# Performance work log

Hardware: AMD Instinct MI355X
Metric: run time of the kernel (lower is better)

Reference implementation:

```python
import jax, jax.numpy as jnp
import numpy as np

DIM = 64
WS = 8    # window_size
SS = 4    # shift_size


def _conv(x, w, pad, groups=1):
    return jax.lax.conv_general_dilated(
        x, w, (1, 1), ((pad, pad), (pad, pad)),
        dimension_numbers=('NCHW', 'OIHW', 'NCHW'),
        feature_group_count=groups)


def _window_partition(x, ws):
    # x: (B, C, H, W) -> (B*Hn*Wn, C, ws, ws), with bottom/right padding
    B, C, H, W = x.shape
    pb = (-H) % ws
    pr = (-W) % ws
    x = jnp.pad(x, ((0, 0), (0, 0), (0, pb), (0, pr)))
    Hp, Wp = H + pb, W + pr
    x = x.reshape(B, C, Hp // ws, ws, Wp // ws, ws).transpose(0, 1, 2, 4, 3, 5)
    return x.reshape(-1, C, ws, ws)


def _window_reverse(wins, ws, H, W):
    pb = (-H) % ws
    pr = (-W) % ws
    Hp, Wp = H + pb, W + pr
    B = wins.shape[0] // ((Hp // ws) * (Wp // ws))
    x = wins.reshape(B, -1, Hp // ws, Wp // ws, ws, ws).transpose(0, 1, 2, 4, 3, 5)
    x = x.reshape(B, -1, Hp, Wp)
    return x[:, :, :H, :W]


def _create_mask(H, W, ws, ss):
    # Swin-style additive mask, computed statically with numpy
    Hp = int(np.ceil(H / ws)) * ws
    Wp = int(np.ceil(W / ws)) * ws
    m = np.zeros((Hp, Wp), dtype=np.float32)
    slices = (slice(0, -ws), slice(-ws, -ss), slice(-ss, None))
    cnt = 0
    for hs in slices:
        for wsl in slices:
            m[hs, wsl] = cnt
            cnt += 1
    mw = m.reshape(Hp // ws, ws, Wp // ws, ws).transpose(0, 2, 1, 3).reshape(-1, ws * ws)
    diff = mw[:, None, :] - mw[:, :, None]
    return jnp.asarray(np.where(diff != 0, -100.0, 0.0).astype(np.float32))


def _l2norm(x):
    # matches torch F.normalize(dim=-1, eps=1e-12)
    return x / jnp.maximum(jnp.linalg.norm(x, axis=-1, keepdims=True), 1e-12)


def _win_attn(xw, w_qkv, w_dw, w_proj, ws, mask, b):
    # xw: (N, C, ws, ws) windows
    C = xw.shape[1]
    qkv = _conv(_conv(xw, w_qkv, 0), w_dw, 1, groups=3 * C)
    q, k, v = jnp.split(qkv, 3, axis=1)
    N = q.shape[0]
    hw = ws * ws
    q = _l2norm(q.reshape(N, C, hw))
    k = _l2norm(k.reshape(N, C, hw))
    v = v.reshape(N, C, hw)
    attn = jnp.einsum('nci,ncj->nij', q, k) / ws  # (N, hw, hw)
    if mask is not None:
        attn = (attn.reshape(b, -1, hw, hw) + mask[None]).reshape(-1, hw, hw)
    attn = jax.nn.softmax(attn, axis=-1)
    out = jnp.einsum('nci,nij->ncj', v, attn).reshape(N, C, ws, ws)
    return _conv(out, w_proj, 1)


def _forward(x, w_qkv0, w_dw0, w_proj0, w_qkv1, w_dw1, w_proj1):
    b, c, h, w = x.shape
    # pass 1: unshifted windows
    xw = _window_partition(x, WS)
    out = _win_attn(xw, w_qkv0, w_dw0, w_proj0, WS, None, b)
    out = _window_reverse(out, WS, h, w)
    # pass 2: shifted windows with Swin mask
    shift = jnp.roll(out, (-SS, -SS), axis=(2, 3))
    sw = _window_partition(shift, WS)
    mask = _create_mask(h, w, WS, SS)
    out = _win_attn(sw, w_qkv1, w_dw1, w_proj1, WS, mask, b)
    out = _window_reverse(out, WS, h, w)
    return jnp.roll(out, (SS, SS), axis=(2, 3))


def setup_inputs() -> dict:
    key = jax.random.key(0)
    ks = jax.random.split(key, 7)
    C = DIM
    s = 0.05
    return {
        'x': jax.random.normal(ks[0], (8, C, 256, 256), jnp.float32),
        'w_qkv0': jax.random.normal(ks[1], (3 * C, C, 1, 1), jnp.float32) * s,
        'w_dw0': jax.random.normal(ks[2], (3 * C, 1, 3, 3), jnp.float32) * s,
        'w_proj0': jax.random.normal(ks[3], (C, C, 3, 3), jnp.float32) * s,
        'w_qkv1': jax.random.normal(ks[4], (3 * C, C, 1, 1), jnp.float32) * s,
        'w_dw1': jax.random.normal(ks[5], (3 * C, 1, 3, 3), jnp.float32) * s,
        'w_proj1': jax.random.normal(ks[6], (C, C, 3, 3), jnp.float32) * s,
    }


def reference(x, w_qkv0, w_dw0, w_proj0, w_qkv1, w_dw1, w_proj1):
    return _forward(x, w_qkv0, w_dw0, w_proj0, w_qkv1, w_dw1, w_proj1)
```

## Files before the change

### kernel.cpp

```cpp
#include <hip/hip_runtime.h>


typedef __attribute__((ext_vector_type(8))) short bf8;
typedef __attribute__((ext_vector_type(4))) float f32x4;
#define MFMA(a, b, c) __builtin_amdgcn_mfma_f32_16x16x32_bf16(a, b, c, 0, 0, 0)

__device__ __forceinline__ int xkey(int p) { return ((p >> 3) ^ p) & 7; }
__device__ __forceinline__ int xswz(int p, int c) { return p * 64 + (c ^ (xkey(p) << 3)); }
__device__ __forceinline__ int kswz(int r, int c) {
    return r * 32 + (c ^ ((((r >> 3) ^ (r >> 1)) & 3) << 3));
}
__device__ __forceinline__ int sswz(int ch, int p) {
    return ch * 64 + (p ^ (((ch >> 1) & 7) << 2));
}
__device__ __forceinline__ int jswz(int ch, int p) {
    return ch * 64 + (p ^ (((ch >> 1) & 7) << 3));
}

__device__ __forceinline__ unsigned cvtpk(float a, float b) {
    unsigned r;
    asm("v_cvt_pk_bf16_f32 %0, %1, %2" : "=v"(r) : "v"(a), "v"(b));
    return r;
}

__device__ __forceinline__ void bsplit(float f, short& h, short& l) {
    unsigned u = __float_as_uint(f);
    unsigned hb = (u + 0x7FFFu + ((u >> 16) & 1u)) >> 16;
    float hf = __uint_as_float(hb << 16);
    float r = f - hf;
    unsigned u2 = __float_as_uint(r);
    unsigned lb = (u2 + 0x7FFFu + ((u2 >> 16) & 1u)) >> 16;
    h = (short)hb; l = (short)lb;
}
__device__ __forceinline__ void bsplit2(float a, float b, unsigned& hw, unsigned& lw) {
    hw = cvtpk(a, b);
    float ra = a - __uint_as_float(hw << 16);
    float rb = b - __uint_as_float(hw & 0xFFFF0000u);
    lw = cvtpk(ra, rb);
}

__global__ void k_fq(const float* __restrict__ wq, short* __restrict__ oh, short* __restrict__ ol) {
    int bx = blockIdx.x;
    int kk = bx / 12, tt = bx % 12;
    int tid = threadIdx.x;
    int lane = tid >> 3, j = tid & 7;
    int oc = tt * 16 + (lane & 15);
    int ic = kk * 32 + ((lane >> 4) << 3) + j;
    short h, l; bsplit(wq[oc * 64 + ic], h, l);
    oh[bx * 512 + tid] = h; ol[bx * 512 + tid] = l;
}
__global__ void k_fp(const float* __restrict__ wp, short* __restrict__ oh, short* __restrict__ ol) {
    int bx = blockIdx.x;
    int tap = bx >> 3, kk = (bx >> 2) & 1, tt = bx & 3;
    int tid = threadIdx.x;
    int lane = tid >> 3, j = tid & 7;
    int oc = tt * 16 + (lane & 15);
    int ic = kk * 32 + ((lane >> 4) << 3) + j;
    short h, l; bsplit(wp[(oc * 64 + ic) * 9 + tap], h, l);
    oh[bx * 512 + tid] = h; ol[bx * 512 + tid] = l;
}

__device__ __forceinline__ void dw_one(const float* scr, const float* wd,
                                       int ch, int row, float o[8]) {
    float w9[9];
    #pragma unroll
    for (int tp = 0; tp < 9; ++tp) w9[tp] = wd[tp];
    float e[3][10];
    #pragma unroll
    for (int k3 = 0; k3 < 3; ++k3) {
        int rr = row - 1 + k3;
        e[k3][0] = 0.f; e[k3][9] = 0.f;
        if ((unsigned)rr < 8u) {
            float4 a = *(const float4*)&scr[sswz(ch, rr * 8)];
            float4 b = *(const float4*)&scr[sswz(ch, rr * 8 + 4)];
            e[k3][1] = a.x; e[k3][2] = a.y; e[k3][3] = a.z; e[k3][4] = a.w;
            e[k3][5] = b.x; e[k3][6] = b.y; e[k3][7] = b.z; e[k3][8] = b.w;
        } else {
            #pragma unroll
            for (int q2 = 1; q2 < 9; ++q2) e[k3][q2] = 0.f;
        }
    }
    #pragma unroll
    for (int s = 0; s < 8; ++s) {
        float a = 0.f;
        #pragma unroll
        for (int k3 = 0; k3 < 3; ++k3)
            #pragma unroll
            for (int dx = 0; dx < 3; ++dx)
                a = fmaf(w9[k3 * 3 + dx], e[k3][s + dx], a);
        o[s] = a;
    }
}

__device__ __forceinline__ float norm8(const float d[8]) {
    float ss = 0.f;
    #pragma unroll
    for (int s = 0; s < 8; ++s) ss = fmaf(d[s], d[s], ss);
    ss += __shfl_xor(ss, 1); ss += __shfl_xor(ss, 2); ss += __shfl_xor(ss, 4);
    return fmaxf(sqrtf(ss), 1e-12f);
}

__device__ __forceinline__ void p2_chunk32(const short* XTh, const short* XTl,
                                           const short* bqh, const short* bql,
                                           float* scr, int chunk,
                                           int mh, int nh, int col, int quad, int qo8, int lane)
{
    f32x4 acc[2];
    #pragma unroll
    for (int mt = 0; mt < 2; ++mt) acc[mt] = (f32x4){0.f, 0.f, 0.f, 0.f};
    #pragma unroll
    for (int kk = 0; kk < 2; ++kk) {
        bf8 Ah[2], Al[2];
        #pragma unroll
        for (int mt = 0; mt < 2; ++mt) {
            int row = (mh * 2 + mt) * 16 + col;
            int ad = row * 64 + ((kk * 32 + qo8) ^ (xkey(row) << 3));
            Ah[mt] = *(const bf8*)&XTh[ad];
            Al[mt] = *(const bf8*)&XTl[ad];
        }
        int tt = chunk * 2 + nh;
        bf8 Bh = *(const bf8*)&bqh[((kk * 12 + tt) * 64 + lane) * 8];
        bf8 Bl = *(const bf8*)&bql[((kk * 12 + tt) * 64 + lane) * 8];
        #pragma unroll
        for (int mt = 0; mt < 2; ++mt) {
            acc[mt] = MFMA(Ah[mt], Bh, acc[mt]);
            acc[mt] = MFMA(Ah[mt], Bl, acc[mt]);
            acc[mt] = MFMA(Al[mt], Bh, acc[mt]);
        }
    }
    #pragma unroll
    for (int mt = 0; mt < 2; ++mt) {
        int ocl = nh * 16 + col;
        int p0 = (mh * 2 + mt) * 16 + quad * 4;
        *(f32x4*)&scr[sswz(ocl, p0)] = acc[mt];
    }
}

__global__ __launch_bounds__(256, 4)
void k_fused(const float* __restrict__ in,
             const short* __restrict__ bqh, const short* __restrict__ bql,
             const float* __restrict__ wdw,
             const short* __restrict__ bph, const short* __restrict__ bpl,
             float* __restrict__ out, int shift, int use_mask, int roll)
{
    __shared__ __align__(16) char smem[32768];
    short* XTh = (short*)smem;
    short* XTl = (short*)(smem + 8192);
    short* K0h = (short*)(smem + 16384);
    short* K0l = (short*)(smem + 20480);
    short* K1h = (short*)(smem + 24576);
    short* K1l = (short*)(smem + 28672);
    float* scr = (float*)(smem + 24576);
    short* vbh = (short*)(smem + 16384);
    short* vbl = (short*)(smem + 20480);
    short* PTf = (short*)(smem + 24576);
    short* PTg = (short*)(smem + 28672);
    float* projo = (float*)(smem + 16384);

    const int tid = threadIdx.x, lane = tid & 63, wv = tid >> 6;
    const int col = lane & 15, quad = lane >> 4, qo8 = quad * 8;
    const int mh = wv & 1, nh = wv >> 1;
    const int ch = tid >> 3, rrow = tid & 7;
    const int n = blockIdx.x;
    const int b = n >> 10, c = (n >> 4) & 63, t = n & 15;
    const size_t base = ((size_t)(b * 64 + c)) << 16;

    #pragma unroll
    for (int k = 0; k < 16; k += 2) {
        int o0 = tid + k * 256, o1 = o0 + 256;
        int hi0 = o0 >> 11, r0 = (o0 >> 8) & 7, lo0 = (o0 >> 3) & 31, s0 = o0 & 7;
        int hi1 = o1 >> 11, r1 = (o1 >> 8) & 7, lo1 = (o1 >> 3) & 31, s1 = o1 & 7;
        float v0 = in[base + (size_t)(((t * 16 + hi0 * 8 + r0) + shift) & 255) * 256
                           + (((lo0 * 8 + s0) + shift) & 255)];
        float v1 = in[base + (size_t)(((t * 16 + hi1 * 8 + r1) + shift) & 255) * 256
                           + (((lo1 * 8 + s1) + shift) & 255)];
        unsigned hw, lw; bsplit2(v0, v1, hw, lw);
        int ad0 = xswz(r0 * 8 + s0, hi0 * 32 + lo0);
        int ad1 = xswz(r1 * 8 + s1, hi1 * 32 + lo1);
        XTh[ad0] = (short)hw; XTh[ad1] = (short)(hw >> 16);
        XTl[ad0] = (short)lw; XTl[ad1] = (short)(lw >> 16);
    }
    __syncthreads();

    unsigned qAh[4], qAl[4], qBh[4], qBl[4];
    unsigned vAh[4], vAl[4], vBh[4], vBl[4];
    float nqA, nqB;

    p2_chunk32(XTh, XTl, bqh, bql, scr, 0, mh, nh, col, quad, qo8, lane);
    __syncthreads();
    {
        float dq[8];
        dw_one(scr, wdw + ch * 9, ch, rrow, dq);
        nqA = norm8(dq);
        #pragma unroll
        for (int q2 = 0; q2 < 4; ++q2) bsplit2(dq[2 * q2], dq[2 * q2 + 1], qAh[q2], qAl[q2]);
    }
    __syncthreads();
    p2_chunk32(XTh, XTl, bqh, bql, scr, 1, mh, nh, col, quad, qo8, lane);
    __syncthreads();
    {
        float dq[8];
        dw_one(scr, wdw + (32 + ch) * 9, ch, rrow, dq);
        nqB = norm8(dq);
        #pragma unroll
        for (int q2 = 0; q2 < 4; ++q2) bsplit2(dq[2 * q2], dq[2 * q2 + 1], qBh[q2], qBl[q2]);
    }
    __syncthreads();
    p2_chunk32(XTh, XTl, bqh, bql, scr, 4, mh, nh, col, quad, qo8, lane);
    __syncthreads();
    {
        float dv[8];
        dw_one(scr, wdw + (128 + ch) * 9, ch, rrow, dv);
        #pragma unroll
        for (int q2 = 0; q2 < 4; ++q2) bsplit2(dv[2 * q2], dv[2 * q2 + 1], vAh[q2], vAl[q2]);
    }
    __syncthreads();
    p2_chunk32(XTh, XTl, bqh, bql, scr, 5, mh, nh, col, quad, qo8, lane);
    __syncthreads();
    {
        float dv[8];
        dw_one(scr, wdw + (160 + ch) * 9, ch, rrow, dv);
        #pragma unroll
        for (int q2 = 0; q2 < 4; ++q2) bsplit2(dv[2 * q2], dv[2 * q2 + 1], vBh[q2], vBl[q2]);
    }
    __syncthreads();
    p2_chunk32(XTh, XTl, bqh, bql, scr, 2, mh, nh, col, quad, qo8, lane);
    __syncthreads();
    {
        float dk[8];
        dw_one(scr, wdw + (64 + ch) * 9, ch, rrow, dk);
        float sc = 0.125f / (nqA * norm8(dk));
        #pragma unroll
        for (int s = 0; s < 8; ++s) dk[s] *= sc;
        #pragma unroll
        for (int s0 = 0; s0 < 8; s0 += 2) {
            unsigned hw, lw; bsplit2(dk[s0], dk[s0 + 1], hw, lw);
            int p0 = rrow * 8 + s0;
            int a0 = kswz(p0, ch), a1 = kswz(p0 + 1, ch);
            K0h[a0] = (short)hw; K0h[a1] = (short)(hw >> 16);
            K0l[a0] = (short)lw; K0l[a1] = (short)(lw >> 16);
        }
    }
    __syncthreads();
    p2_chunk32(XTh, XTl, bqh, bql, scr, 3, mh, nh, col, quad, qo8, lane);
    __syncthreads();
    unsigned k1h[4], k1l[4];
    {
        float dk[8];
        dw_one(scr, wdw + (96 + ch) * 9, ch, rrow, dk);
        float sc = 0.125f / (nqB * norm8(dk));
        #pragma unroll
        for (int s = 0; s < 8; ++s) dk[s] *= sc;
        #pragma unroll
        for (int q2 = 0; q2 < 4; ++q2) bsplit2(dk[2 * q2], dk[2 * q2 + 1], k1h[q2], k1l[q2]);
    }
    #pragma unroll
    for (int q2 = 0; q2 < 4; ++q2) {
        int p0 = rrow * 8 + 2 * q2;
        int a0 = xswz(p0, ch), a1 = xswz(p0 + 1, ch);
        XTh[a0] = (short)qAh[q2]; XTh[a1] = (short)(qAh[q2] >> 16);
        XTl[a0] = (short)qAl[q2]; XTl[a1] = (short)(qAl[q2] >> 16);
        int cg = 32 + ch;
        int b0 = xswz(p0, cg), b1 = xswz(p0 + 1, cg);
        XTh[b0] = (short)qBh[q2]; XTh[b1] = (short)(qBh[q2] >> 16);
        XTl[b0] = (short)qBl[q2]; XTl[b1] = (short)(qBl[q2] >> 16);
    }
    __syncthreads();
    #pragma unroll
    for (int q2 = 0; q2 < 4; ++q2) {
        int p0 = rrow * 8 + 2 * q2;
        int a0 = kswz(p0, ch), a1 = kswz(p0 + 1, ch);
        K1h[a0] = (short)k1h[q2]; K1h[a1] = (short)(k1h[q2] >> 16);
        K1l[a0] = (short)k1l[q2]; K1l[a1] = (short)(k1l[q2] >> 16);
    }
    __syncthreads();

    f32x4 at[4];
    #pragma unroll
    for (int nt = 0; nt < 4; ++nt) at[nt] = (f32x4){0.f, 0.f, 0.f, 0.f};
    {
        bf8 Ah[2], Al[2];
        #pragma unroll
        for (int kk = 0; kk < 2; ++kk) {
            int row = wv * 16 + col;
            int ad = row * 64 + ((kk * 32 + qo8) ^ (xkey(row) << 3));
            Ah[kk] = *(const bf8*)&XTh[ad];
            Al[kk] = *(const bf8*)&XTl[ad];
        }
        #pragma unroll
        for (int kk = 0; kk < 2; ++kk) {
            const short* Bph = kk ? K1h : K0h;
            const short* Bpl = kk ? K1l : K0l;
            #pragma unroll
            for (int nt = 0; nt < 4; ++nt) {
                int rowB = nt * 16 + col;
                int ad = kswz(rowB, qo8);
                bf8 Bh = *(const bf8*)&Bph[ad];
                bf8 Bl = *(const bf8*)&Bpl[ad];
                at[nt] = MFMA(Ah[kk], Bh, at[nt]);
                at[nt] = MFMA(Ah[kk], Bl, at[nt]);
                at[nt] = MFMA(Al[kk], Bh, at[nt]);
            }
        }
    }
    if (use_mask) {
        const int widx = n & 1023;
        const int hn_m = widx >> 5, wn_m = widx & 31;
        #pragma unroll
        for (int nt = 0; nt < 4; ++nt) {
            int j = nt * 16 + col;
            int rj = ((hn_m == 31) ? (((j >> 3) < 4) ? 1 : 2) : 0) * 3
                   + ((wn_m == 31) ? (((j & 7) < 4) ? 1 : 2) : 0);
            #pragma unroll
            for (int rg = 0; rg < 4; ++rg) {
                int i = wv * 16 + quad * 4 + rg;
                int ri = ((hn_m == 31) ? (((i >> 3) < 4) ? 1 : 2) : 0) * 3
                       + ((wn_m == 31) ? (((i & 7) < 4) ? 1 : 2) : 0);
                if (ri != rj) at[nt][rg] = at[nt][rg] - 100.f;
            }
        }
    }
    unsigned Ph[4][2], Pl[4][2];
    {
        float Pv[4][4];
        #pragma unroll
        for (int rg = 0; rg < 4; ++rg) {
            float m = fmaxf(fmaxf(at[0][rg], at[1][rg]), fmaxf(at[2][rg], at[3][rg]));
            m = fmaxf(m, __shfl_xor(m, 1)); m = fmaxf(m, __shfl_xor(m, 2));
            m = fmaxf(m, __shfl_xor(m, 4)); m = fmaxf(m, __shfl_xor(m, 8));
            float e0 = __expf(at[0][rg] - m), e1 = __expf(at[1][rg] - m);
            float e2 = __expf(at[2][rg] - m), e3 = __expf(at[3][rg] - m);
            float s = e0 + e1 + e2 + e3;
            s += __shfl_xor(s, 1); s += __shfl_xor(s, 2);
            s += __shfl_xor(s, 4); s += __shfl_xor(s, 8);
            float is = 1.0f / s;
            Pv[0][rg] = e0 * is; Pv[1][rg] = e1 * is; Pv[2][rg] = e2 * is; Pv[3][rg] = e3 * is;
        }
        #pragma unroll
        for (int nt = 0; nt < 4; ++nt)
            #pragma unroll
            for (int rp = 0; rp < 2; ++rp)
                bsplit2(Pv[nt][2 * rp], Pv[nt][2 * rp + 1], Ph[nt][rp], Pl[nt][rp]);
    }
    __syncthreads();

    f32x4 av[2][2];
    #pragma unroll
    for (int mt = 0; mt < 2; ++mt)
        #pragma unroll
        for (int nt = 0; nt < 2; ++nt) av[mt][nt] = (f32x4){0.f, 0.f, 0.f, 0.f};
    #pragma unroll
    for (int ih = 0; ih < 2; ++ih) {
        if ((rrow >> 2) == ih) {
            int rl = rrow & 3;
            int adA = kswz(ch, rl * 8);
            *(uint4*)&vbh[adA] = (uint4){vAh[0], vAh[1], vAh[2], vAh[3]};
            *(uint4*)&vbl[adA] = (uint4){vAl[0], vAl[1], vAl[2], vAl[3]};
            int adB = kswz(32 + ch, rl * 8);
            *(uint4*)&vbh[adB] = (uint4){vBh[0], vBh[1], vBh[2], vBh[3]};
            *(uint4*)&vbl[adB] = (uint4){vBl[0], vBl[1], vBl[2], vBl[3]};
        }
        if ((wv >> 1) == ih) {
            #pragma unroll
            for (int nt = 0; nt < 4; ++nt) {
                int j = nt * 16 + col;
                #pragma unroll
                for (int rp = 0; rp < 2; ++rp) {
                    int il = (wv & 1) * 16 + quad * 4 + 2 * rp;
                    int ad = kswz(j, il);
                    *(unsigned*)&PTf[ad] = Ph[nt][rp];
                    *(unsigned*)&PTg[ad] = Pl[nt][rp];
                }
            }
        }
        __syncthreads();
        {
            bf8 Ah[2], Al[2], Bh[2], Bl[2];
            #pragma unroll
            for (int mt = 0; mt < 2; ++mt) {
                int row = (mh * 2 + mt) * 16 + col;
                int ad = kswz(row, qo8);
                Ah[mt] = *(const bf8*)&vbh[ad];
                Al[mt] = *(const bf8*)&vbl[ad];
            }
            #pragma unroll
            for (int nt = 0; nt < 2; ++nt) {
                int rowB = (nh * 2 + nt) * 16 + col;
                int ad = kswz(rowB, qo8);
                Bh[nt] = *(const bf8*)&PTf[ad];
                Bl[nt] = *(const bf8*)&PTg[ad];
            }
            #pragma unroll
            for (int mt = 0; mt < 2; ++mt)
                #pragma unroll
                for (int nt = 0; nt < 2; ++nt) {
                    av[mt][nt] = MFMA(Ah[mt], Bh[nt], av[mt][nt]);
                    av[mt][nt] = MFMA(Ah[mt], Bl[nt], av[mt][nt]);
                    av[mt][nt] = MFMA(Al[mt], Bh[nt], av[mt][nt]);
                }
        }
        __syncthreads();
    }
    #pragma unroll
    for (int nt = 0; nt < 2; ++nt) {
        int j = (nh * 2 + nt) * 16 + col;
        #pragma unroll
        for (int mt = 0; mt < 2; ++mt) {
            int c0 = (mh * 2 + mt) * 16 + quad * 4;
            #pragma unroll
            for (int rp = 0; rp < 2; ++rp) {
                unsigned hw, lw; bsplit2(av[mt][nt][2 * rp], av[mt][nt][2 * rp + 1], hw, lw);
                int ad = j * 64 + ((c0 + 2 * rp) ^ (xkey(j) << 3));
                *(unsigned*)&XTh[ad] = hw;
                *(unsigned*)&XTl[ad] = lw;
            }
        }
    }
    if (tid < 32) ((unsigned*)(smem + 16384))[tid] = 0u;
    __syncthreads();

    {
        f32x4 ap[2][2];
        #pragma unroll
        for (int mt = 0; mt < 2; ++mt)
            #pragma unroll
            for (int nt = 0; nt < 2; ++nt) ap[mt][nt] = (f32x4){0.f, 0.f, 0.f, 0.f};
        const int smc = col & 7;
        #pragma unroll 1
        for (int tap = 0; tap < 9; ++tap) {
            int dy = (tap >= 6) ? 1 : ((tap >= 3) ? 0 : -1);
            int dx = tap - (dy + 1) * 3 - 1;
            int ra_h[2], ra_l[2];
            #pragma unroll
            for (int mt = 0; mt < 2; ++mt) {
                int rr = (mh * 2 + mt) * 2 + (col >> 3) + dy;
                int ss = smc + dx;
                bool ok = ((unsigned)rr < 8u) && ((unsigned)ss < 8u);
                int row = rr * 8 + ss;
                ra_h[mt] = ok ? row : 128;
                ra_l[mt] = ok ? row : 64;
            }
            #pragma unroll
            for (int kk = 0; kk < 2; ++kk) {
                bf8 Bh[2], Bl[2], Ah[2], Al[2];
                #pragma unroll
                for (int nt = 0; nt < 2; ++nt) {
                    int bi = (((tap * 2 + kk) * 4 + (nh * 2 + nt)) * 64 + lane) * 8;
                    Bh[nt] = *(const bf8*)&bph[bi];
                    Bl[nt] = *(const bf8*)&bpl[bi];
                }
                #pragma unroll
                for (int mt = 0; mt < 2; ++mt) {
                    int adh = ra_h[mt] * 64 + ((kk * 32 + qo8) ^ (xkey(ra_h[mt]) << 3));
                    int adl = ra_l[mt] * 64 + ((kk * 32 + qo8) ^ (xkey(ra_l[mt]) << 3));
                    Ah[mt] = *(const bf8*)&XTh[adh];
                    Al[mt] = *(const bf8*)&XTl[adl];
                }
                #pragma unroll
                for (int mt = 0; mt < 2; ++mt)
                    #pragma unroll
                    for (int nt = 0; nt < 2; ++nt) {
                        ap[mt][nt] = MFMA(Ah[mt], Bh[nt], ap[mt][nt]);
                        ap[mt][nt] = MFMA(Ah[mt], Bl[nt], ap[mt][nt]);
                        ap[mt][nt] = MFMA(Al[mt], Bh[nt], ap[mt][nt]);
                    }
            }
        }
        __syncthreads();
        #pragma unroll
        for (int nt = 0; nt < 2; ++nt) {
            int oc = (nh * 2 + nt) * 16 + col;
            #pragma unroll
            for (int mt = 0; mt < 2; ++mt) {
                int p0 = (mh * 2 + mt) * 16 + quad * 4;
                *(f32x4*)&projo[jswz(oc, p0)] = ap[mt][nt];
            }
        }
    }
    __syncthreads();

    #pragma unroll
    for (int k = 0; k < 16; ++k) {
        int o = tid + k * 256;
        int hi = o >> 11, r = (o >> 8) & 7, lo = (o >> 3) & 31, s = o & 7;
        int c2 = hi * 32 + lo;
        float v = projo[jswz(c2, r * 8 + s)];
        int h2 = t * 16 + hi * 8 + r, w2 = lo * 8 + s;
        out[base + (size_t)((h2 + roll) & 255) * 256 + ((w2 + roll) & 255)] = v;
    }
}

extern "C" void kernel_launch(void* const* d_in, const int* in_sizes, int n_in,
                              void* d_out, int out_size, void* d_ws, size_t ws_size,
                              hipStream_t stream)
{
    const float* x      = (const float*)d_in[0];
    const float* wqkv0  = (const float*)d_in[1];
    const float* wdw0   = (const float*)d_in[2];
    const float* wproj0 = (const float*)d_in[3];
    const float* wqkv1  = (const float*)d_in[4];
    const float* wdw1   = (const float*)d_in[5];
    const float* wproj1 = (const float*)d_in[6];
    float* out = (float*)d_out;

    float* tmp = (float*)d_ws;
    short* fb  = (short*)(tmp + 33554432);
    short* bq0h = fb;
    short* bq0l = fb + 12288;
    short* bq1h = fb + 24576;
    short* bq1l = fb + 36864;
    short* bp0h = fb + 49152;
    short* bp0l = fb + 86016;
    short* bp1h = fb + 122880;
    short* bp1l = fb + 159744;

    hipLaunchKernelGGL(k_fq, dim3(24), dim3(512), 0, stream, wqkv0, bq0h, bq0l);
    hipLaunchKernelGGL(k_fq, dim3(24), dim3(512), 0, stream, wqkv1, bq1h, bq1l);
    hipLaunchKernelGGL(k_fp, dim3(72), dim3(512), 0, stream, wproj0, bp0h, bp0l);
    hipLaunchKernelGGL(k_fp, dim3(72), dim3(512), 0, stream, wproj1, bp1h, bp1l);

    hipLaunchKernelGGL(k_fused, dim3(8192), dim3(256), 0, stream,
                       x, bq0h, bq0l, wdw0, bp0h, bp0l, tmp, 0, 0, 0);
    hipLaunchKernelGGL(k_fused, dim3(8192), dim3(256), 0, stream,
                       tmp, bq1h, bq1l, wdw1, bp1h, bp1l, out, 4, 1, 4);
}
```

Baseline: 619.4 us.

## Double-buffer QKV chunk scratch, templatize shift/mask/roll, hoist swizzle address math

The QKV projection chunks now alternate between two shared-memory scratch buffers, so the MFMA for the next chunk overlaps the depthwise conv of the previous one and about half the barriers go away. The K0 tile is kept in registers and written to shared memory at the end instead of mid-sequence. Shift, mask and roll become template parameters, so the unshifted pass uses contiguous indexing and dead branches are removed. Swizzled LDS addresses are hoisted out of the kk loops and use XOR, at the cost of more live registers under the 4-wave occupancy bound.

```diff
diff --git a/kernel.cpp b/kernel.cpp
--- a/kernel.cpp
+++ b/kernel.cpp
@@ -108,13 +108,18 @@
     f32x4 acc[2];
     #pragma unroll
     for (int mt = 0; mt < 2; ++mt) acc[mt] = (f32x4){0.f, 0.f, 0.f, 0.f};
+    int ad0[2];
+    #pragma unroll
+    for (int mt = 0; mt < 2; ++mt) {
+        int row = (mh * 2 + mt) * 16 + col;
+        ad0[mt] = row * 64 + (qo8 ^ (xkey(row) << 3));
+    }
     #pragma unroll
     for (int kk = 0; kk < 2; ++kk) {
         bf8 Ah[2], Al[2];
         #pragma unroll
         for (int mt = 0; mt < 2; ++mt) {
-            int row = (mh * 2 + mt) * 16 + col;
-            int ad = row * 64 + ((kk * 32 + qo8) ^ (xkey(row) << 3));
+            int ad = ad0[mt] ^ (kk << 5);
             Ah[mt] = *(const bf8*)&XTh[ad];
             Al[mt] = *(const bf8*)&XTl[ad];
         }
@@ -136,21 +141,23 @@
     }
 }
 
+template<int SHIFT, int MASK, int ROLL>
 __global__ __launch_bounds__(256, 4)
 void k_fused(const float* __restrict__ in,
              const short* __restrict__ bqh, const short* __restrict__ bql,
              const float* __restrict__ wdw,
              const short* __restrict__ bph, const short* __restrict__ bpl,
-             float* __restrict__ out, int shift, int use_mask, int roll)
+             float* __restrict__ out)
 {
     __shared__ __align__(16) char smem[32768];
     short* XTh = (short*)smem;
     short* XTl = (short*)(smem + 8192);
+    float* bufA = (float*)(smem + 16384);
+    float* bufB = (float*)(smem + 24576);
     short* K0h = (short*)(smem + 16384);
     short* K0l = (short*)(smem + 20480);
     short* K1h = (short*)(smem + 24576);
     short* K1l = (short*)(smem + 28672);
-    float* scr = (float*)(smem + 24576);
     short* vbh = (short*)(smem + 16384);
     short* vbl = (short*)(smem + 20480);
     short* PTf = (short*)(smem + 24576);
@@ -168,13 +175,21 @@
     #pragma unroll
     for (int k = 0; k < 16; k += 2) {
         int o0 = tid + k * 256, o1 = o0 + 256;
+        float v0, v1;
+        if (SHIFT == 0) {
+            const float* src = in + base + (size_t)t * 4096;
+            v0 = src[o0]; v1 = src[o1];
+        } else {
+            int hi0 = o0 >> 11, r0 = (o0 >> 8) & 7, lo0 = (o0 >> 3) & 31, s0 = o0 & 7;
+            int hi1 = o1 >> 11, r1 = (o1 >> 8) & 7, lo1 = (o1 >> 3) & 31, s1 = o1 & 7;
+            v0 = in[base + (size_t)(((t * 16 + hi0 * 8 + r0) + SHIFT) & 255) * 256
+                         + (((lo0 * 8 + s0) + SHIFT) & 255)];
+            v1 = in[base + (size_t)(((t * 16 + hi1 * 8 + r1) + SHIFT) & 255) * 256
+                         + (((lo1 * 8 + s1) + SHIFT) & 255)];
+        }
+        unsigned hw, lw; bsplit2(v0, v1, hw, lw);
         int hi0 = o0 >> 11, r0 = (o0 >> 8) & 7, lo0 = (o0 >> 3) & 31, s0 = o0 & 7;
         int hi1 = o1 >> 11, r1 = (o1 >> 8) & 7, lo1 = (o1 >> 3) & 31, s1 = o1 & 7;
-        float v0 = in[base + (size_t)(((t * 16 + hi0 * 8 + r0) + shift) & 255) * 256
-                           + (((lo0 * 8 + s0) + shift) & 255)];
-        float v1 = in[base + (size_t)(((t * 16 + hi1 * 8 + r1) + shift) & 255) * 256
-                           + (((lo1 * 8 + s1) + shift) & 255)];
-        unsigned hw, lw; bsplit2(v0, v1, hw, lw);
         int ad0 = xswz(r0 * 8 + s0, hi0 * 32 + lo0);
         int ad1 = xswz(r1 * 8 + s1, hi1 * 32 + lo1);
         XTh[ad0] = (short)hw; XTh[ad1] = (short)(hw >> 16);
@@ -184,86 +199,78 @@
 
     unsigned qAh[4], qAl[4], qBh[4], qBl[4];
     unsigned vAh[4], vAl[4], vBh[4], vBl[4];
+    unsigned k0h[4], k0l[4], k1h[4], k1l[4];
     float nqA, nqB;
 
-    p2_chunk32(XTh, XTl, bqh, bql, scr, 0, mh, nh, col, quad, qo8, lane);
-    __syncthreads();
-    {
-        float dq[8];
-        dw_one(scr, wdw + ch * 9, ch, rrow, dq);
-        nqA = norm8(dq);
-        #pragma unroll
-        for (int q2 = 0; q2 < 4; ++q2) bsplit2(dq[2 * q2], dq[2 * q2 + 1], qAh[q2], qAl[q2]);
-    }
-    __syncthreads();
-    p2_chunk32(XTh, XTl, bqh, bql, scr, 1, mh, nh, col, quad, qo8, lane);
-    __syncthreads();
-    {
-        float dq[8];
-        dw_one(scr, wdw + (32 + ch) * 9, ch, rrow, dq);
-        nqB = norm8(dq);
-        #pragma unroll
-        for (int q2 = 0; q2 < 4; ++q2) bsplit2(dq[2 * q2], dq[2 * q2 + 1], qBh[q2], qBl[q2]);
-    }
-    __syncthreads();
-    p2_chunk32(XTh, XTl, bqh, bql, scr, 4, mh, nh, col, quad, qo8, lane);
-    __syncthreads();
-    {
-        float dv[8];
-        dw_one(scr, wdw + (128 + ch) * 9, ch, rrow, dv);
-        #pragma unroll
-        for (int q2 = 0; q2 < 4; ++q2) bsplit2(dv[2 * q2], dv[2 * q2 + 1], vAh[q2], vAl[q2]);
-    }
-    __syncthreads();
-    p2_chunk32(XTh, XTl, bqh, bql, scr, 5, mh, nh, col, quad, qo8, lane);
-    __syncthreads();
-    {
-        float dv[8];
-        dw_one(scr, wdw + (160 + ch) * 9, ch, rrow, dv);
-        #pragma unroll
-        for (int q2 = 0; q2 < 4; ++q2) bsplit2(dv[2 * q2], dv[2 * q2 + 1], vBh[q2], vBl[q2]);
-    }
-    __syncthreads();
-    p2_chunk32(XTh, XTl, bqh, bql, scr, 2, mh, nh, col, quad, qo8, lane);
-    __syncthreads();
-    {
-        float dk[8];
-        dw_one(scr, wdw + (64 + ch) * 9, ch, rrow, dk);
-        float sc = 0.125f / (nqA * norm8(dk));
-        #pragma unroll
-        for (int s = 0; s < 8; ++s) dk[s] *= sc;
-        #pragma unroll
-        for (int s0 = 0; s0 < 8; s0 += 2) {
-            unsigned hw, lw; bsplit2(dk[s0], dk[s0 + 1], hw, lw);
-            int p0 = rrow * 8 + s0;
-            int a0 = kswz(p0, ch), a1 = kswz(p0 + 1, ch);
-            K0h[a0] = (short)hw; K0h[a1] = (short)(hw >> 16);
-            K0l[a0] = (short)lw; K0l[a1] = (short)(lw >> 16);
-        }
-    }
-    __syncthreads();
-    p2_chunk32(XTh, XTl, bqh, bql, scr, 3, mh, nh, col, quad, qo8, lane);
-    __syncthreads();
-    unsigned k1h[4], k1l[4];
-    {
-        float dk[8];
-        dw_one(scr, wdw + (96 + ch) * 9, ch, rrow, dk);
-        float sc = 0.125f / (nqB * norm8(dk));
-        #pragma unroll
-        for (int s = 0; s < 8; ++s) dk[s] *= sc;
-        #pragma unroll
-        for (int q2 = 0; q2 < 4; ++q2) bsplit2(dk[2 * q2], dk[2 * q2 + 1], k1h[q2], k1l[q2]);
+    p2_chunk32(XTh, XTl, bqh, bql, bufA, 0, mh, nh, col, quad, qo8, lane);
+    __syncthreads();
+    p2_chunk32(XTh, XTl, bqh, bql, bufB, 1, mh, nh, col, quad, qo8, lane);
+    {
+        float d[8];
+        dw_one(bufA, wdw + ch * 9, ch, rrow, d);
+        nqA = norm8(d);
+        #pragma unroll
+        for (int q2 = 0; q2 < 4; ++q2) bsplit2(d[2 * q2], d[2 * q2 + 1], qAh[q2], qAl[q2]);
+    }
+    __syncthreads();
+    p2_chunk32(XTh, XTl, bqh, bql, bufA, 4, mh, nh, col, quad, qo8, lane);
+    {
+        float d[8];
+        dw_one(bufB, wdw + (32 + ch) * 9, ch, rrow, d);
+        nqB = norm8(d);
+        #pragma unroll
+        for (int q2 = 0; q2 < 4; ++q2) bsplit2(d[2 * q2], d[2 * q2 + 1], qBh[q2], qBl[q2]);
+    }
+    __syncthreads();
+    p2_chunk32(XTh, XTl, bqh, bql, bufB, 5, mh, nh, col, quad, qo8, lane);
+    {
+        float d[8];
+        dw_one(bufA, wdw + (128 + ch) * 9, ch, rrow, d);
+        #pragma unroll
+        for (int q2 = 0; q2 < 4; ++q2) bsplit2(d[2 * q2], d[2 * q2 + 1], vAh[q2], vAl[q2]);
+    }
+    __syncthreads();
+    p2_chunk32(XTh, XTl, bqh, bql, bufA, 2, mh, nh, col, quad, qo8, lane);
+    {
+        float d[8];
+        dw_one(bufB, wdw + (160 + ch) * 9, ch, rrow, d);
+        #pragma unroll
+        for (int q2 = 0; q2 < 4; ++q2) bsplit2(d[2 * q2], d[2 * q2 + 1], vBh[q2], vBl[q2]);
+    }
+    __syncthreads();
+    p2_chunk32(XTh, XTl, bqh, bql, bufB, 3, mh, nh, col, quad, qo8, lane);
+    {
+        float d[8];
+        dw_one(bufA, wdw + (64 + ch) * 9, ch, rrow, d);
+        float sc = 0.125f / (nqA * norm8(d));
+        #pragma unroll
+        for (int s = 0; s < 8; ++s) d[s] *= sc;
+        #pragma unroll
+        for (int q2 = 0; q2 < 4; ++q2) bsplit2(d[2 * q2], d[2 * q2 + 1], k0h[q2], k0l[q2]);
+    }
+    __syncthreads();
+    {
+        float d[8];
+        dw_one(bufB, wdw + (96 + ch) * 9, ch, rrow, d);
+        float sc = 0.125f / (nqB * norm8(d));
+        #pragma unroll
+        for (int s = 0; s < 8; ++s) d[s] *= sc;
+        #pragma unroll
+        for (int q2 = 0; q2 < 4; ++q2) bsplit2(d[2 * q2], d[2 * q2 + 1], k1h[q2], k1l[q2]);
     }
     #pragma unroll
     for (int q2 = 0; q2 < 4; ++q2) {
         int p0 = rrow * 8 + 2 * q2;
-        int a0 = xswz(p0, ch), a1 = xswz(p0 + 1, ch);
-        XTh[a0] = (short)qAh[q2]; XTh[a1] = (short)(qAh[q2] >> 16);
-        XTl[a0] = (short)qAl[q2]; XTl[a1] = (short)(qAl[q2] >> 16);
+        int a0 = kswz(p0, ch), a1 = kswz(p0 + 1, ch);
+        K0h[a0] = (short)k0h[q2]; K0h[a1] = (short)(k0h[q2] >> 16);
+        K0l[a0] = (short)k0l[q2]; K0l[a1] = (short)(k0l[q2] >> 16);
+        int x0 = xswz(p0, ch), x1 = xswz(p0 + 1, ch);
+        XTh[x0] = (short)qAh[q2]; XTh[x1] = (short)(qAh[q2] >> 16);
+        XTl[x0] = (short)qAl[q2]; XTl[x1] = (short)(qAl[q2] >> 16);
         int cg = 32 + ch;
-        int b0 = xswz(p0, cg), b1 = xswz(p0 + 1, cg);
-        XTh[b0] = (short)qBh[q2]; XTh[b1] = (short)(qBh[q2] >> 16);
-        XTl[b0] = (short)qBl[q2]; XTl[b1] = (short)(qBl[q2] >> 16);
+        int y0 = xswz(p0, cg), y1 = xswz(p0 + 1, cg);
+        XTh[y0] = (short)qBh[q2]; XTh[y1] = (short)(qBh[q2] >> 16);
+        XTl[y0] = (short)qBl[q2]; XTl[y1] = (short)(qBl[q2] >> 16);
     }
     __syncthreads();
     #pragma unroll
@@ -280,10 +287,11 @@
     for (int nt = 0; nt < 4; ++nt) at[nt] = (f32x4){0.f, 0.f, 0.f, 0.f};
     {
         bf8 Ah[2], Al[2];
+        int rowA = wv * 16 + col;
+        int adA0 = rowA * 64 + (qo8 ^ (xkey(rowA) << 3));
         #pragma unroll
         for (int kk = 0; kk < 2; ++kk) {
-            int row = wv * 16 + col;
-            int ad = row * 64 + ((kk * 32 + qo8) ^ (xkey(row) << 3));
+            int ad = adA0 ^ (kk << 5);
             Ah[kk] = *(const bf8*)&XTh[ad];
             Al[kk] = *(const bf8*)&XTl[ad];
         }
@@ -303,7 +311,7 @@
             }
         }
     }
-    if (use_mask) {
+    if (MASK) {
         const int widx = n & 1023;
         const int hn_m = widx >> 5, wn_m = widx & 31;
         #pragma unroll
@@ -430,15 +438,17 @@
         for (int tap = 0; tap < 9; ++tap) {
             int dy = (tap >= 6) ? 1 : ((tap >= 3) ? 0 : -1);
             int dx = tap - (dy + 1) * 3 - 1;
-            int ra_h[2], ra_l[2];
+            int bh0[2], bl0[2];
             #pragma unroll
             for (int mt = 0; mt < 2; ++mt) {
                 int rr = (mh * 2 + mt) * 2 + (col >> 3) + dy;
                 int ss = smc + dx;
                 bool ok = ((unsigned)rr < 8u) && ((unsigned)ss < 8u);
                 int row = rr * 8 + ss;
-                ra_h[mt] = ok ? row : 128;
-                ra_l[mt] = ok ? row : 64;
+                int ra_h = ok ? row : 128;
+                int ra_l = ok ? row : 64;
+                bh0[mt] = ra_h * 64 + (qo8 ^ (xkey(ra_h) << 3));
+                bl0[mt] = ra_l * 64 + (qo8 ^ (xkey(ra_l) << 3));
             }
             #pragma unroll
             for (int kk = 0; kk < 2; ++kk) {
@@ -451,10 +461,8 @@
                 }
                 #pragma unroll
                 for (int mt = 0; mt < 2; ++mt) {
-                    int adh = ra_h[mt] * 64 + ((kk * 32 + qo8) ^ (xkey(ra_h[mt]) << 3));
-                    int adl = ra_l[mt] * 64 + ((kk * 32 + qo8) ^ (xkey(ra_l[mt]) << 3));
-                    Ah[mt] = *(const bf8*)&XTh[adh];
-                    Al[mt] = *(const bf8*)&XTl[adl];
+                    Ah[mt] = *(const bf8*)&XTh[bh0[mt] ^ (kk << 5)];
+                    Al[mt] = *(const bf8*)&XTl[bl0[mt] ^ (kk << 5)];
                 }
                 #pragma unroll
                 for (int mt = 0; mt < 2; ++mt)
@@ -485,8 +493,13 @@
         int hi = o >> 11, r = (o >> 8) & 7, lo = (o >> 3) & 31, s = o & 7;
         int c2 = hi * 32 + lo;
         float v = projo[jswz(c2, r * 8 + s)];
-        int h2 = t * 16 + hi * 8 + r, w2 = lo * 8 + s;
-        out[base + (size_t)((h2 + roll) & 255) * 256 + ((w2 + roll) & 255)] = v;
+        if (ROLL == 0) {
+            float* dst = out + base + (size_t)t * 4096;
+            dst[o] = v;
+        } else {
+            int h2 = t * 16 + hi * 8 + r, w2 = lo * 8 + s;
+            out[base + (size_t)((h2 + ROLL) & 255) * 256 + ((w2 + ROLL) & 255)] = v;
+        }
     }
 }
 
@@ -519,8 +532,8 @@
     hipLaunchKernelGGL(k_fp, dim3(72), dim3(512), 0, stream, wproj0, bp0h, bp0l);
     hipLaunchKernelGGL(k_fp, dim3(72), dim3(512), 0, stream, wproj1, bp1h, bp1l);
 
-    hipLaunchKernelGGL(k_fused, dim3(8192), dim3(256), 0, stream,
-                       x, bq0h, bq0l, wdw0, bp0h, bp0l, tmp, 0, 0, 0);
-    hipLaunchKernelGGL(k_fused, dim3(8192), dim3(256), 0, stream,
-                       tmp, bq1h, bq1l, wdw1, bp1h, bp1l, out, 4, 1, 4);
-}
+    hipLaunchKernelGGL(HIP_KERNEL_NAME(k_fused<0, 0, 0>), dim3(8192), dim3(256), 0, stream,
+                       x, bq0h, bq0l, wdw0, bp0h, bp0l, tmp);
+    hipLaunchKernelGGL(HIP_KERNEL_NAME(k_fused<4, 1, 4>), dim3(8192), dim3(256), 0, stream,
+                       tmp, bq1h, bq1l, wdw1, bp1h, bp1l, out);
+}
```

Result: no change. 610.0 us (-1.5%).
